# Kernel tuning notes

Hardware: AMD Instinct MI355X
Metric: run time of the kernel (lower is better)

The kernel has to match this reference:

```python
import jax, jax.numpy as jnp
import numpy as np

N_NODES = 20000
N_EDGES = 160000
N_GRAPHS = 16
NEG_INF = -1e30


def gcn_conv(x, edge_index, edge_weight, W, b):
    # PyG GCNConv with improved=True: add self-loops with weight 2.0,
    # symmetric degree normalization, linear transform, scatter-add aggregation.
    N = x.shape[0]
    row, col = edge_index[0], edge_index[1]
    loop = jnp.arange(N)
    row = jnp.concatenate([row, loop])
    col = jnp.concatenate([col, loop])
    ew = jnp.concatenate([edge_weight, jnp.full((N,), 2.0, edge_weight.dtype)])
    deg = jax.ops.segment_sum(ew, col, num_segments=N)
    dinv = jnp.where(deg > 0, deg ** -0.5, 0.0)  # deg_inv_sqrt, inf -> 0
    norm = dinv[row] * ew * dinv[col]            # [E+N]
    xl = x @ W                                   # [N, out]
    out = jax.ops.segment_sum(xl[row] * norm[:, None], col, num_segments=N)
    return out + b


def segment_softmax_masked(logits, mask, batch, num_segments):
    # softmax over masked entries, grouped by graph id (torch_geometric softmax
    # after masked_select); unmasked-out positions return 0.
    neg = jnp.asarray(NEG_INF, logits.dtype)
    ml = jnp.where(mask, logits, neg)
    mx = jax.ops.segment_max(ml, batch, num_segments=num_segments)
    ex = jnp.where(mask, jnp.exp(logits - mx[batch]), 0.0)
    s = jax.ops.segment_sum(ex, batch, num_segments=num_segments)
    return ex / jnp.maximum(s[batch], 1e-16)


def setup_inputs() -> dict:
    key = jax.random.key(0)
    ks = jax.random.split(key, 12)
    x = jax.random.normal(ks[0], (N_NODES, 5), dtype=jnp.float32)
    edge_index = jax.random.randint(ks[1], (2, N_EDGES), 0, N_NODES)
    edge_weight = jax.random.uniform(ks[2], (N_EDGES,), dtype=jnp.float32)
    mask = jax.random.randint(ks[3], (N_NODES,), 0, 2).astype(bool)
    batch = jnp.sort(jax.random.randint(ks[4], (N_NODES,), 0, N_GRAPHS))
    # parameters (Glorot-ish scaling)
    W1 = jax.random.normal(ks[5], (5, 1000), dtype=jnp.float32) / np.sqrt(5)
    b1 = jnp.zeros((1000,), jnp.float32)
    W2 = jax.random.normal(ks[6], (1000, 1000), dtype=jnp.float32) / np.sqrt(1000)
    b2 = jnp.zeros((1000,), jnp.float32)
    Wf = jax.random.normal(ks[7], (1000, 1), dtype=jnp.float32) / np.sqrt(1000)
    bf = jnp.zeros((1,), jnp.float32)
    return {"x": x, "edge_weight": edge_weight, "W1": W1, "b1": b1,
            "W2": W2, "b2": b2, "Wf": Wf, "bf": bf,
            "edge_index": edge_index, "mask": mask, "batch": batch}


def reference(x, edge_weight, W1, b1, W2, b2, Wf, bf, edge_index, mask, batch):
    h = jax.nn.relu(gcn_conv(x, edge_index, edge_weight, W1, b1))
    h = jax.nn.relu(gcn_conv(h, edge_index, edge_weight, W2, b2))
    # dropout treated as identity (eval mode) for a deterministic reference
    logits = (h @ Wf + bf)[:, 0]  # [N]
    return segment_softmax_masked(logits, mask, batch, N_GRAPHS)
```

## Files before the change

### kernel.cpp

```cpp
#include <hip/hip_runtime.h>

#define NN 20000
#define NE 160000
#define NG 16
#define KP 1024
#define MT2 160
#define MPAD2 (MT2*128)
#define NBLK 79

typedef __attribute__((ext_vector_type(8))) short bf16x8;
typedef __attribute__((ext_vector_type(4))) float f32x4;

#define GAS __attribute__((address_space(1)))
#define LAS __attribute__((address_space(3)))

__device__ __forceinline__ unsigned short f2bf(float f) {
    unsigned int u = __float_as_uint(f);
    u += 0x7FFFu + ((u >> 16) & 1u);
    return (unsigned short)(u >> 16);
}

__device__ __forceinline__ void gld_lds16(const char* g, char* l) {
    __builtin_amdgcn_global_load_lds((GAS void*)g, (LAS void*)l, 16, 0, 0);
}

__global__ void deg_cnt_kernel(const int* __restrict__ ei, const float* __restrict__ ew,
                               float* deg, int* cnt, const void* __restrict__ mask,
                               int* flags) {
    const int e = blockIdx.x * blockDim.x + threadIdx.x;
    if (e < 5000) {
        const unsigned v = ((const unsigned*)mask)[e];
        if (v > 1u) atomicOr(&flags[0], 1);
        if (v != 0u && v != 0x3F800000u) atomicOr(&flags[1], 1);
    }
    if (e >= NE) return;
    const int c = ei[NE + e];
    atomicAdd(&deg[c], ew[e]);
    atomicAdd(&cnt[c], 1);
}

__global__ __launch_bounds__(256) void partial_w2t_kernel(const int* __restrict__ cnt,
        const float* __restrict__ deg, const void* __restrict__ mask,
        const int* __restrict__ flags, int* __restrict__ mtmp,
        float* __restrict__ dinv, int* __restrict__ bcnt, int* __restrict__ bmsk,
        const float* __restrict__ W2, unsigned short* __restrict__ W2t,
        float* __restrict__ logitsC) {
    const int bid = blockIdx.x;
    const int t = threadIdx.x;
    if (bid < NBLK) {
        const int i = bid * 256 + t;
        const int f0 = flags[0], f1 = flags[1];
        int c = 0, mv = 0;
        if (i < NN) {
            c = cnt[i];
            dinv[i] = 1.0f / sqrtf(2.0f + deg[i]);
            if (f0 == 0)      mv = ((const int*)mask)[i] != 0;
            else if (f1 == 0) mv = ((const unsigned*)mask)[i] != 0u;
            else              mv = ((const unsigned char*)mask)[i] != 0;
            mtmp[i] = mv;
        }
        __shared__ int sc[256], sm[256];
        sc[t] = c; sm[t] = mv;
        __syncthreads();
        for (int off = 128; off; off >>= 1) {
            if (t < off) { sc[t] += sc[t + off]; sm[t] += sm[t + off]; }
            __syncthreads();
        }
        if (t == 0) { bcnt[bid] = sc[0]; bmsk[bid] = sm[0]; }
    } else {
        __shared__ float tile[32][33];
        const int bw = bid - NBLK;
        if (t < 20) logitsC[bw * 20 + t] = 0.0f;
        const int n0 = (bw & 31) * 32;
        const int k0 = (bw >> 5) * 32;
        const int tx = t & 31, ty = t >> 5;
#pragma unroll
        for (int j = 0; j < 4; ++j) {
            const int k = k0 + ty + j * 8;
            const int n = n0 + tx;
            tile[ty + j * 8][tx] = (k < 1000 && n < 1000) ? W2[k * 1000 + n] : 0.0f;
        }
        __syncthreads();
#pragma unroll
        for (int j = 0; j < 4; ++j) {
            const int n = n0 + ty + j * 8;
            const int k = k0 + tx;
            W2t[(size_t)n * KP + k] = f2bf(tile[tx][ty + j * 8]);
        }
    }
}

__global__ __launch_bounds__(256) void apply_kernel(const int* __restrict__ cnt,
        const int* __restrict__ mtmp, const int* __restrict__ bcnt,
        const int* __restrict__ bmsk, const int* __restrict__ batch,
        int* __restrict__ offs, int* __restrict__ perm, int* __restrict__ bc,
        int* __restrict__ nm, int* __restrict__ cursor, float* __restrict__ out) {
    const int b = blockIdx.x, t = threadIdx.x;
    __shared__ int pbc[128], pbm[128];
    if (t < 128) {
        pbc[t] = (t < NBLK) ? bcnt[t] : 0;
        pbm[t] = (t < NBLK) ? bmsk[t] : 0;
    }
    __syncthreads();
    for (int off = 1; off < 128; off <<= 1) {
        int uc = 0, um = 0;
        if (t < 128 && t >= off) { uc = pbc[t - off]; um = pbm[t - off]; }
        __syncthreads();
        if (t < 128) { pbc[t] += uc; pbm[t] += um; }
        __syncthreads();
    }
    if (b == 0 && t == 0) nm[0] = pbm[NBLK - 1];
    const int bco = (b == 0) ? 0 : pbc[b - 1];
    const int bmo = (b == 0) ? 0 : pbm[b - 1];
    const int i = b * 256 + t;
    const int c  = (i < NN) ? cnt[i]  : 0;
    const int mv = (i < NN) ? mtmp[i] : 0;
    __shared__ int sc[256], sm[256];
    sc[t] = c; sm[t] = mv;
    __syncthreads();
    for (int off = 1; off < 256; off <<= 1) {
        const int uc = (t >= off) ? sc[t - off] : 0;
        const int um = (t >= off) ? sm[t - off] : 0;
        __syncthreads();
        sc[t] += uc; sm[t] += um;
        __syncthreads();
    }
    if (i < NN) {
        cursor[i] = 0;
        out[i] = 0.0f;
        offs[i] = bco + sc[t] - c;
        if (mv) {
            const int pos = bmo + sm[t] - 1;
            perm[pos] = i;
            bc[pos] = batch[i];
        }
    }
}

__global__ void scatter_kernel(const int* __restrict__ ei, const float* __restrict__ ew,
                               const float* __restrict__ dinv, const int* __restrict__ offs,
                               int* cursor, int* __restrict__ ssrc, float* __restrict__ snorm) {
    const int e = blockIdx.x * blockDim.x + threadIdx.x;
    if (e >= NE) return;
    const int r = ei[e], c = ei[NE + e];
    const int pos = atomicAdd(&cursor[c], 1);
    const int idx = offs[c] + pos;
    ssrc[idx] = r;
    snorm[idx] = dinv[r] * ew[e] * dinv[c];
}

__global__ __launch_bounds__(256) void axf_kernel(const float* __restrict__ x,
        const int* __restrict__ ssrc, const float* __restrict__ snorm,
        const int* __restrict__ offs, const int* __restrict__ cnt,
        const float* __restrict__ dinv, float* __restrict__ Axf) {
    const int i = blockIdx.x * blockDim.x + threadIdx.x;
    if (i >= NN) return;
    float a0=0,a1=0,a2=0,a3=0,a4=0;
    const int s0 = offs[i], n = cnt[i];
    for (int e = s0; e < s0 + n; ++e) {
        const int r = ssrc[e];
        const float w = snorm[e];
        const float* xr = x + r * 5;
        a0 += w*xr[0]; a1 += w*xr[1]; a2 += w*xr[2]; a3 += w*xr[3]; a4 += w*xr[4];
    }
    const float wl = 2.0f * dinv[i] * dinv[i];
    const float* xi = x + i * 5;
    a0 += wl*xi[0]; a1 += wl*xi[1]; a2 += wl*xi[2]; a3 += wl*xi[3]; a4 += wl*xi[4];
    float* o = Axf + i * 5;
    o[0]=a0; o[1]=a1; o[2]=a2; o[3]=a3; o[4]=a4;
}

__global__ __launch_bounds__(256) void aggW1_kernel(const float* __restrict__ Axf,
        const float* __restrict__ W1, const float* __restrict__ b1,
        const int* __restrict__ ssrc, const float* __restrict__ snorm,
        const int* __restrict__ offs, const int* __restrict__ cnt,
        const float* __restrict__ dinv, const int* __restrict__ perm,
        const int* __restrict__ nm, unsigned short* __restrict__ G) {
    const int tid = threadIdx.x;
    const int wv = tid >> 6;
    const int lane = tid & 63;
    const int half = wv & 1;
    const int jbase = blockIdx.x * 8 + (wv >> 1) * 4;
    const int nmv = nm[0];
    const int npad = (nmv + 127) & ~127;
    if (jbase >= npad) return;

    const int c0 = half * 512 + lane * 8;
    float w1r[5][8], bbr[8];
#pragma unroll
    for (int q = 0; q < 2; ++q) {
        const int c = c0 + q * 4;
        const bool v = (c <= 996);
#pragma unroll
        for (int f = 0; f < 5; ++f) {
            const float4 w4 = v ? *(const float4*)(W1 + f * 1000 + c)
                                : make_float4(0.f, 0.f, 0.f, 0.f);
            w1r[f][q*4+0] = w4.x; w1r[f][q*4+1] = w4.y;
            w1r[f][q*4+2] = w4.z; w1r[f][q*4+3] = w4.w;
        }
        const float4 b4 = v ? *(const float4*)(b1 + c) : make_float4(0.f, 0.f, 0.f, 0.f);
        bbr[q*4+0] = b4.x; bbr[q*4+1] = b4.y; bbr[q*4+2] = b4.z; bbr[q*4+3] = b4.w;
    }

    int iv[4], s0a[4], na[4]; float dva[4];
#pragma unroll
    for (int d = 0; d < 4; ++d) {
        const int j = jbase + d;
        iv[d] = (j < nmv) ? perm[j] : -1;
    }
#pragma unroll
    for (int d = 0; d < 4; ++d) {
        if (iv[d] >= 0) { s0a[d] = offs[iv[d]]; na[d] = cnt[iv[d]]; dva[d] = dinv[iv[d]]; }
        else            { s0a[d] = 0; na[d] = -1; dva[d] = 0.f; }
    }

#pragma unroll
    for (int d = 0; d < 4; ++d) {
        const int j = jbase + d;
        float acc[8];
#pragma unroll
        for (int k = 0; k < 8; ++k) acc[k] = 0.f;
        const int i = iv[d];
        if (i >= 0) {
            const int s0 = s0a[d], n = na[d];
            const int total = n + 1;
            for (int base = 0; base < total; base += 64) {
                const int m = (total - base < 64) ? (total - base) : 64;
                float a0=0.f, a1=0.f, a2=0.f, a3=0.f, a4=0.f, we=0.f;
                if (lane < m) {
                    const int idx = base + lane;
                    int r;
                    if (idx < n) { r = ssrc[s0 + idx]; we = snorm[s0 + idx]; }
                    else         { r = i; we = 2.0f * dva[d] * dva[d]; }
                    const float* axr = Axf + r * 5;
                    a0 = axr[0]; a1 = axr[1]; a2 = axr[2]; a3 = axr[3]; a4 = axr[4];
                }
#pragma unroll 2
                for (int e = 0; e < m; ++e) {
                    const float s0v = __shfl(a0, e);
                    const float s1v = __shfl(a1, e);
                    const float s2v = __shfl(a2, e);
                    const float s3v = __shfl(a3, e);
                    const float s4v = __shfl(a4, e);
                    const float swv = __shfl(we, e);
#pragma unroll
                    for (int k = 0; k < 8; ++k) {
                        const float z = bbr[k] + s0v * w1r[0][k] + s1v * w1r[1][k]
                                      + s2v * w1r[2][k] + s3v * w1r[3][k] + s4v * w1r[4][k];
                        acc[k] += swv * fmaxf(z, 0.f);
                    }
                }
            }
        }
        bf16x8 pk;
#pragma unroll
        for (int k = 0; k < 8; ++k) pk[k] = (short)f2bf(acc[k]);
        *(bf16x8*)(G + (size_t)j * KP + c0) = pk;
    }
}

__global__ __launch_bounds__(256) void gemm_kernel(const unsigned short* __restrict__ A,
                                                   const unsigned short* __restrict__ B,
                                                   const float* __restrict__ b2,
                                                   const float* __restrict__ Wf,
                                                   const int* __restrict__ nm,
                                                   float* __restrict__ logitsC) {
    __shared__ unsigned short As[4096];
    __shared__ unsigned short Bs[4096];
    const int tid = threadIdx.x;
    __shared__ int s_nm;
    if (tid == 0) s_nm = nm[0];
    __syncthreads();
    const int nmv = s_nm;
    const int mstrips = (nmv + 127) >> 7;
    const int bid = blockIdx.x;
    const int tm = (bid >> 6) * 8 + (bid & 7);
    const int tn = (bid >> 3) & 7;
    if (tm >= mstrips) return;
    const int lane = tid & 63;
    const int wv = tid >> 6;
    const int wr = wv >> 1, wc = wv & 1;

    const int chunk = ((tid & 3) ^ ((tid >> 3) & 3)) * 16;
    const int rsub = tid >> 2;
    const char* Ag = (const char*)(A + (size_t)(tm * 128 + rsub) * KP) + chunk;
    const char* Bg = (const char*)(B + (size_t)(tn * 128 + rsub) * KP) + chunk;
    char* AsW = (char*)As + wv * 1024;
    char* BsW = (char*)Bs + wv * 1024;

    f32x4 acc[4][4];
#pragma unroll
    for (int i = 0; i < 4; ++i)
#pragma unroll
        for (int j = 0; j < 4; ++j) acc[i][j] = (f32x4){0.f, 0.f, 0.f, 0.f};

    const int m = lane & 15;
    const int quad = lane >> 4;
    const int sw = quad ^ ((m >> 1) & 3);
    const int aoff = (wr * 64 + m) * 64 + sw * 16;
    const int boff = (wc * 64 + m) * 64 + sw * 16;

    for (int kk = 0; kk < KP; kk += 32) {
        __syncthreads();
        const int kb = kk * 2;
        gld_lds16(Ag + kb,             AsW);
        gld_lds16(Ag + kb + 64 * 2048, AsW + 4096);
        gld_lds16(Bg + kb,             BsW);
        gld_lds16(Bg + kb + 64 * 2048, BsW + 4096);
        __syncthreads();
        bf16x8 af[4], bfv[4];
#pragma unroll
        for (int mt = 0; mt < 4; ++mt)
            af[mt] = *(const bf16x8*)((const char*)As + aoff + mt * 1024);
#pragma unroll
        for (int nt = 0; nt < 4; ++nt)
            bfv[nt] = *(const bf16x8*)((const char*)Bs + boff + nt * 1024);
#pragma unroll
        for (int mt = 0; mt < 4; ++mt)
#pragma unroll
            for (int nt = 0; nt < 4; ++nt)
                acc[mt][nt] = __builtin_amdgcn_mfma_f32_16x16x32_bf16(af[mt], bfv[nt], acc[mt][nt], 0, 0, 0);
    }

    const int col0 = tn * 128 + wc * 64 + m;
    const int row00 = tm * 128 + wr * 64 + quad * 4;
#pragma unroll
    for (int mt = 0; mt < 4; ++mt) {
        float ps0 = 0.f, ps1 = 0.f, ps2 = 0.f, ps3 = 0.f;
#pragma unroll
        for (int nt = 0; nt < 4; ++nt) {
            const int c = col0 + nt * 16;
            const float bbv = (c < 1000) ? b2[c] : 0.0f;
            const float wfv = (c < 1000) ? Wf[c] : 0.0f;
            ps0 += fmaxf(acc[mt][nt][0] + bbv, 0.f) * wfv;
            ps1 += fmaxf(acc[mt][nt][1] + bbv, 0.f) * wfv;
            ps2 += fmaxf(acc[mt][nt][2] + bbv, 0.f) * wfv;
            ps3 += fmaxf(acc[mt][nt][3] + bbv, 0.f) * wfv;
        }
#pragma unroll
        for (int msk = 1; msk < 16; msk <<= 1) {
            ps0 += __shfl_xor(ps0, msk);
            ps1 += __shfl_xor(ps1, msk);
            ps2 += __shfl_xor(ps2, msk);
            ps3 += __shfl_xor(ps3, msk);
        }
        if (m == 0) {
            const int row = row00 + mt * 16;
            if (row + 0 < nmv) atomicAdd(&logitsC[row + 0], ps0);
            if (row + 1 < nmv) atomicAdd(&logitsC[row + 1], ps1);
            if (row + 2 < nmv) atomicAdd(&logitsC[row + 2], ps2);
            if (row + 3 < nmv) atomicAdd(&logitsC[row + 3], ps3);
        }
    }
}

__global__ __launch_bounds__(256) void softmax_kernel(const float* __restrict__ logitsC,
        const int* __restrict__ perm, const int* __restrict__ bc,
        const int* __restrict__ nm, float* __restrict__ out) {
    const int g = blockIdx.x;
    const int t = threadIdx.x;
    __shared__ int s_lo, s_hi;
    __shared__ float red[4];
    __shared__ float sval;
    if (t == 0) {
        const int nmv = nm[0];
        int lo = 0, hi = nmv;
        while (lo < hi) { const int mid = (lo + hi) >> 1; if (bc[mid] < g) lo = mid + 1; else hi = mid; }
        s_lo = lo;
        int lo2 = lo, hi2 = nmv;
        while (lo2 < hi2) { const int mid = (lo2 + hi2) >> 1; if (bc[mid] < g + 1) lo2 = mid + 1; else hi2 = mid; }
        s_hi = lo2;
    }
    __syncthreads();
    const int lo = s_lo, hi = s_hi;
    float mx = -1e30f;
    for (int i = lo + t; i < hi; i += 256) mx = fmaxf(mx, logitsC[i]);
    for (int off = 32; off; off >>= 1) mx = fmaxf(mx, __shfl_down(mx, off));
    if ((t & 63) == 0) red[t >> 6] = mx;
    __syncthreads();
    if (t == 0) sval = fmaxf(fmaxf(red[0], red[1]), fmaxf(red[2], red[3]));
    __syncthreads();
    mx = sval;
    __syncthreads();
    float sm = 0.f;
    for (int i = lo + t; i < hi; i += 256) sm += expf(logitsC[i] - mx);
    for (int off = 32; off; off >>= 1) sm += __shfl_down(sm, off);
    if ((t & 63) == 0) red[t >> 6] = sm;
    __syncthreads();
    if (t == 0) sval = red[0] + red[1] + red[2] + red[3];
    __syncthreads();
    const float inv = 1.0f / fmaxf(sval, 1e-16f);
    for (int i = lo + t; i < hi; i += 256)
        out[perm[i]] = expf(logitsC[i] - mx) * inv;
}

extern "C" void kernel_launch(void* const* d_in, const int* in_sizes, int n_in,
                              void* d_out, int out_size, void* d_ws, size_t ws_size,
                              hipStream_t stream) {
    (void)in_sizes; (void)n_in; (void)out_size; (void)ws_size;
    const float* x   = (const float*)d_in[0];
    const float* ew  = (const float*)d_in[1];
    const float* W1  = (const float*)d_in[2];
    const float* b1  = (const float*)d_in[3];
    const float* W2  = (const float*)d_in[4];
    const float* b2  = (const float*)d_in[5];
    const float* Wf  = (const float*)d_in[6];
    const int*   ei  = (const int*)d_in[8];
    const void*  mask  = d_in[9];
    const int*   batch = (const int*)d_in[10];
    float* out = (float*)d_out;

    char* p = (char*)d_ws;
    auto carve = [&](size_t bytes) { char* q = p; p += (bytes + 255) & ~(size_t)255; return q; };
    char* zbase = p;
    float* deg     = (float*)carve(NN * 4);
    int*   cnt     = (int*)carve(NN * 4);
    int*   flags   = (int*)carve(256);
    size_t zspan = (size_t)(p - zbase);
    int*   cursor  = (int*)carve(NN * 4);
    float* logitsC = (float*)carve(MPAD2 * 4);
    int*   offs   = (int*)carve(NN * 4);
    float* dinv   = (float*)carve(NN * 4);
    int*   mtmp   = (int*)carve(NN * 4);
    int*   perm   = (int*)carve(NN * 4);
    int*   bc     = (int*)carve(NN * 4);
    int*   bcnt   = (int*)carve(NBLK * 4);
    int*   bmsk   = (int*)carve(NBLK * 4);
    int*   nmp    = (int*)carve(256);
    int*   ssrc   = (int*)carve(NE * 4);
    float* snorm  = (float*)carve(NE * 4);
    float* Axf    = (float*)carve(NN * 5 * 4);
    unsigned short* W2t = (unsigned short*)carve((size_t)KP * KP * 2);
    unsigned short* G   = (unsigned short*)carve((size_t)MPAD2 * KP * 2);

    hipMemsetAsync(zbase, 0, zspan, stream);
    hipLaunchKernelGGL(deg_cnt_kernel,     dim3(625),       dim3(256), 0, stream, ei, ew, deg, cnt, mask, flags);
    hipLaunchKernelGGL(partial_w2t_kernel, dim3(NBLK+1024), dim3(256), 0, stream, cnt, deg, mask, flags, mtmp, dinv, bcnt, bmsk, W2, W2t, logitsC);
    hipLaunchKernelGGL(apply_kernel,       dim3(NBLK),      dim3(256), 0, stream, cnt, mtmp, bcnt, bmsk, batch, offs, perm, bc, nmp, cursor, out);
    hipLaunchKernelGGL(scatter_kernel,     dim3(625),       dim3(256), 0, stream, ei, ew, dinv, offs, cursor, ssrc, snorm);
    hipLaunchKernelGGL(axf_kernel,         dim3(79),        dim3(256), 0, stream, x, ssrc, snorm, offs, cnt, dinv, Axf);
    hipLaunchKernelGGL(aggW1_kernel,       dim3(MPAD2/8),   dim3(256), 0, stream, Axf, W1, b1, ssrc, snorm, offs, cnt, dinv, perm, nmp, G);
    hipLaunchKernelGGL(gemm_kernel,        dim3(MT2*8),     dim3(256), 0, stream, G, W2t, b2, Wf, nmp, logitsC);
    hipLaunchKernelGGL(softmax_kernel,     dim3(NG),        dim3(256), 0, stream, logitsC, perm, bc, nmp, out);
}
```

Before: 198.5 us.

## Multi-buffer GEMM LDS tiles with a four-stage async prefetch pipeline

Replaces the single-buffered LDS load/compute loop in the bf16 MFMA GEMM with a four-buffer ring, prefetching three k-steps ahead through direct global-to-LDS loads. Explicit vmcnt waits plus raw s_barrier replace the two __syncthreads per iteration, so global loads overlap MFMA work. LDS use per block rises fourfold (64KB), which may reduce occupancy. Correctness depends on the hand-counted vmcnt thresholds.

```diff
diff --git a/kernel.cpp b/kernel.cpp
--- a/kernel.cpp
+++ b/kernel.cpp
@@ -265,8 +265,8 @@
                                                    const float* __restrict__ Wf,
                                                    const int* __restrict__ nm,
                                                    float* __restrict__ logitsC) {
-    __shared__ unsigned short As[4096];
-    __shared__ unsigned short Bs[4096];
+    __shared__ unsigned short As[4 * 4096];
+    __shared__ unsigned short Bs[4 * 4096];
     const int tid = threadIdx.x;
     __shared__ int s_nm;
     if (tid == 0) s_nm = nm[0];
@@ -300,27 +300,42 @@
     const int aoff = (wr * 64 + m) * 64 + sw * 16;
     const int boff = (wc * 64 + m) * 64 + sw * 16;
 
-    for (int kk = 0; kk < KP; kk += 32) {
-        __syncthreads();
-        const int kb = kk * 2;
-        gld_lds16(Ag + kb,             AsW);
-        gld_lds16(Ag + kb + 64 * 2048, AsW + 4096);
-        gld_lds16(Bg + kb,             BsW);
-        gld_lds16(Bg + kb + 64 * 2048, BsW + 4096);
-        __syncthreads();
+#define STAGE(t32_, b_) do {                                       \
+        const int kb_ = (t32_) * 64;                               \
+        char* a_  = AsW + (b_) * 8192;                             \
+        char* bb_ = BsW + (b_) * 8192;                             \
+        gld_lds16(Ag + kb_,             a_);                       \
+        gld_lds16(Ag + kb_ + 64 * 2048, a_ + 4096);                \
+        gld_lds16(Bg + kb_,             bb_);                      \
+        gld_lds16(Bg + kb_ + 64 * 2048, bb_ + 4096);               \
+    } while (0)
+
+    STAGE(0, 0); STAGE(1, 1); STAGE(2, 2);
+
+    for (int t32 = 0; t32 < 32; ++t32) {
+        const int b = t32 & 3;
+        if (t32 < 30)       asm volatile("s_waitcnt vmcnt(8)" ::: "memory");
+        else if (t32 == 30) asm volatile("s_waitcnt vmcnt(4)" ::: "memory");
+        else                asm volatile("s_waitcnt vmcnt(0)" ::: "memory");
+        __builtin_amdgcn_s_barrier();
+        const char* Ab = (const char*)As + b * 8192;
+        const char* Bb = (const char*)Bs + b * 8192;
         bf16x8 af[4], bfv[4];
 #pragma unroll
         for (int mt = 0; mt < 4; ++mt)
-            af[mt] = *(const bf16x8*)((const char*)As + aoff + mt * 1024);
+            af[mt] = *(const bf16x8*)(Ab + aoff + mt * 1024);
 #pragma unroll
         for (int nt = 0; nt < 4; ++nt)
-            bfv[nt] = *(const bf16x8*)((const char*)Bs + boff + nt * 1024);
+            bfv[nt] = *(const bf16x8*)(Bb + boff + nt * 1024);
 #pragma unroll
         for (int mt = 0; mt < 4; ++mt)
 #pragma unroll
             for (int nt = 0; nt < 4; ++nt)
                 acc[mt][nt] = __builtin_amdgcn_mfma_f32_16x16x32_bf16(af[mt], bfv[nt], acc[mt][nt], 0, 0, 0);
-    }
+        __builtin_amdgcn_s_barrier();
+        if (t32 + 3 < 32) STAGE(t32 + 3, (t32 + 3) & 3);
+    }
+#undef STAGE
 
     const int col0 = tn * 128 + wc * 64 + m;
     const int row00 = tm * 128 + wr * 64 + quad * 4;
```

Result: slower. 213.5 us (+7.5%).
